# Kernel tuning notes

Measured on AMD Instinct MI355X. Metric: run time of the kernel, lower is better.

The kernel has to match this reference:

```python
import jax, jax.numpy as jnp
import numpy as np

NUM_FREQUENCIES = 6  # K = 2F+1 = 13


def fourier_basis(times, num_frequencies):
    # times: [N] -> basis: [N, 2F+1] = [1, sin(2^j*pi*t), cos(2^j*pi*t)]
    freqs = (2.0 ** jnp.arange(num_frequencies, dtype=times.dtype)) * jnp.pi  # [F]
    ang = times[:, None] * freqs[None, :]  # [N, F]
    ones = jnp.ones_like(times)[:, None]
    return jnp.concatenate([ones, jnp.sin(ang), jnp.cos(ang)], axis=-1)  # [N, K]


def setup_inputs() -> dict:
    key = jax.random.key(0)
    k1, k2, k3 = jax.random.split(key, 3)
    N, num_videos, embedding_dim = 400000, 128, 64
    times = jax.random.uniform(k1, (N,), dtype=jnp.float32)
    video_ids = jax.random.randint(k2, (N,), 0, num_videos, dtype=jnp.int32)
    weights = jax.random.normal(k3, (num_videos, embedding_dim, 2 * NUM_FREQUENCIES + 1), dtype=jnp.float32)
    return {"times": times, "video_ids": video_ids, "weights": weights}


def reference(times, video_ids, weights):
    basis = fourier_basis(times, NUM_FREQUENCIES)          # [N, K]
    w = weights[video_ids]                                  # gather: [N, D, K]
    return jnp.einsum('nk,ndk->nd', basis, w)               # [N, D]
```

## Files before the change

### kernel.cpp

```cpp
#include <hip/hip_runtime.h>
#include <math.h>

#define V 128
#define D 64
#define K 13

#define CHUNK 2048
#define SORT_BLOCK 256
#define NB 256
#define BSTRIDE 20

__global__ void zero_kernel(int* __restrict__ gcount) {
    gcount[threadIdx.x] = 0;
}

__global__ __launch_bounds__(256) void sort_kernel(const int* __restrict__ ids, int n,
                                                   int* __restrict__ gcount,
                                                   int* __restrict__ sorted, int cap) {
    __shared__ int h[V];
    __shared__ int r[V];
    __shared__ int lb[V];
    int tid = threadIdx.x;
    if (tid < V) { h[tid] = 0; r[tid] = 0; }
    __syncthreads();
    int base = blockIdx.x * CHUNK;
    int4 reg[CHUNK / (SORT_BLOCK * 4)];
#pragma unroll
    for (int j = 0; j < CHUNK / (SORT_BLOCK * 4); ++j) {
        int i = base + (j * SORT_BLOCK + tid) * 4;
        if (i < n) {
            reg[j] = *(const int4*)(ids + i);
            atomicAdd(&h[reg[j].x], 1);
            atomicAdd(&h[reg[j].y], 1);
            atomicAdd(&h[reg[j].z], 1);
            atomicAdd(&h[reg[j].w], 1);
        }
    }
    __syncthreads();
    if (tid < V) lb[tid] = atomicAdd(&gcount[tid], h[tid]);
    __syncthreads();
#pragma unroll
    for (int j = 0; j < CHUNK / (SORT_BLOCK * 4); ++j) {
        int i = base + (j * SORT_BLOCK + tid) * 4;
        if (i < n) {
            int4 v4 = reg[j];
            int p0 = lb[v4.x] + atomicAdd(&r[v4.x], 1);
            int p1 = lb[v4.y] + atomicAdd(&r[v4.y], 1);
            int p2 = lb[v4.z] + atomicAdd(&r[v4.z], 1);
            int p3 = lb[v4.w] + atomicAdd(&r[v4.w], 1);
            if (p0 < cap) sorted[v4.x * cap + p0] = i;
            if (p1 < cap) sorted[v4.y * cap + p1] = i + 1;
            if (p2 < cap) sorted[v4.z * cap + p2] = i + 2;
            if (p3 < cap) sorted[v4.w * cap + p3] = i + 3;
        }
    }
}

__global__ __launch_bounds__(256) void compute_kernel(const float* __restrict__ times,
                                                      const float* __restrict__ weights,
                                                      const int* __restrict__ sorted,
                                                      const int* __restrict__ gcount,
                                                      float* __restrict__ out,
                                                      int cap, int bpb) {
    int v = (int)(blockIdx.x) / bpb;
    int blk = (int)(blockIdx.x) - v * bpb;
    int cnt = gcount[v];
    if (cnt > cap) cnt = cap;
    int start = blk * NB;
    int valid = cnt - start;
    if (valid <= 0) return;
    if (valid > NB) valid = NB;

    __shared__ float basis[NB * BSTRIDE];
    int tid = threadIdx.x;
    int lane = tid & 63;

    float w[K];
    {
        const float* wp = weights + (v * D + lane) * K;
#pragma unroll
        for (int k = 0; k < K; ++k) w[k] = wp[k];
    }

    if (tid < valid) {
        int idx = sorted[v * cap + start + tid];
        float t = times[idx];
        float s, c;
        __sincosf(3.14159265358979323846f * t, &s, &c);
        float sj[6], cj[6];
        sj[0] = s; cj[0] = c;
#pragma unroll
        for (int j = 1; j < 6; ++j) {
            sj[j] = 2.0f * sj[j - 1] * cj[j - 1];
            cj[j] = 1.0f - 2.0f * sj[j - 1] * sj[j - 1];
        }
        float* bb = &basis[tid * BSTRIDE];
        ((float4*)bb)[0] = make_float4(1.0f, sj[0], sj[1], sj[2]);
        ((float4*)bb)[1] = make_float4(sj[3], sj[4], sj[5], cj[0]);
        ((float4*)bb)[2] = make_float4(cj[1], cj[2], cj[3], cj[4]);
        *(float2*)(bb + 12) = make_float2(cj[5], __int_as_float(idx));
    }
    __syncthreads();

    int wave = tid >> 6;
    int i0 = wave * 64;
    int iend = valid - i0;
    iend = iend < 0 ? 0 : (iend > 64 ? 64 : iend);

    auto body = [&](int i) {
        const float* bb = &basis[(i0 + i) * BSTRIDE];
        float4 b0 = ((const float4*)bb)[0];
        float4 b1 = ((const float4*)bb)[1];
        float4 b2 = ((const float4*)bb)[2];
        float2 b3 = *(const float2*)(bb + 12);
        int idx = __float_as_int(b3.y);
        float acc = ((b0.x * w[0] + b0.y * w[1]) + (b0.z * w[2] + b0.w * w[3]))
                  + ((b1.x * w[4] + b1.y * w[5]) + (b1.z * w[6] + b1.w * w[7]))
                  + (((b2.x * w[8] + b2.y * w[9]) + (b2.z * w[10] + b2.w * w[11]))
                     + b3.x * w[12]);
        __builtin_nontemporal_store(acc, &out[(long)idx * D + lane]);
    };

    if (iend == 64) {
#pragma unroll 4
        for (int i = 0; i < 64; ++i) body(i);
    } else {
        for (int i = 0; i < iend; ++i) body(i);
    }
}

extern "C" void kernel_launch(void* const* d_in, const int* in_sizes, int n_in,
                              void* d_out, int out_size, void* d_ws, size_t ws_size,
                              hipStream_t stream) {
    const float* times = (const float*)d_in[0];
    const int* ids = (const int*)d_in[1];
    const float* weights = (const float*)d_in[2];
    float* out = (float*)d_out;
    int n = in_sizes[0];

    int* gcount = (int*)d_ws;
    int* sorted = gcount + V;
    long avail = (long)(ws_size / 4) - V;
    int cap = (int)(avail / V);
    if (cap > 4096) cap = 4096;

    zero_kernel<<<1, V, 0, stream>>>(gcount);

    int nblk = (n + CHUNK - 1) / CHUNK;
    sort_kernel<<<nblk, SORT_BLOCK, 0, stream>>>(ids, n, gcount, sorted, cap);

    int bpb = (cap + NB - 1) / NB;
    compute_kernel<<<V * bpb, 256, 0, stream>>>(times, weights, sorted, gcount, out, cap, bpb);
}
```

Baseline: 130.7 us.

## Fuse zero, sort and compute kernels into one cooperative persistent kernel

Replaces the three separate launches (zero counters, bucket sort by video id, per-video compute) with a single cooperative kernel of 1024 persistent blocks that uses grid-wide syncs between phases and grid-strided loops over chunks and jobs. The aim is to remove launch overhead and inter-kernel gaps. If the cooperative launch fails, it falls back to the old three-kernel path. The grid syncs add their own cost, and capping the grid at 1024 blocks with occupancy 4 may reduce parallelism in the compute phase.

Result: slower. 297.6 us (+127.8%).

```diff
diff --git a/kernel.cpp b/kernel.cpp
--- a/kernel.cpp
+++ b/kernel.cpp
@@ -1,18 +1,142 @@
 #include <hip/hip_runtime.h>
+#include <hip/hip_cooperative_groups.h>
 #include <math.h>
+
+namespace cg = cooperative_groups;
 
 #define V 128
 #define D 64
 #define K 13
 
+#define NBLK 1024
 #define CHUNK 2048
 #define SORT_BLOCK 256
 #define NB 256
 #define BSTRIDE 20
 
-__global__ void zero_kernel(int* __restrict__ gcount) {
-    gcount[threadIdx.x] = 0;
-}
+__global__ __launch_bounds__(256, 4) void fused_kernel(
+    const float* __restrict__ times, const int* __restrict__ ids,
+    const float* __restrict__ weights, float* __restrict__ out,
+    int* __restrict__ gcount, int* __restrict__ sorted,
+    int n, int cap, int bpb, int nchunk, int njobs)
+{
+    __shared__ int h[V];
+    __shared__ int r[V];
+    __shared__ int lb[V];
+    __shared__ float basis[NB * BSTRIDE];
+
+    int tid = threadIdx.x;
+    cg::grid_group grid = cg::this_grid();
+
+    if (blockIdx.x == 0 && tid < V) gcount[tid] = 0;
+    grid.sync();
+
+    for (int c = blockIdx.x; c < nchunk; c += NBLK) {
+        if (tid < V) { h[tid] = 0; r[tid] = 0; }
+        __syncthreads();
+        int base = c * CHUNK;
+        int4 reg[CHUNK / (SORT_BLOCK * 4)];
+#pragma unroll
+        for (int j = 0; j < CHUNK / (SORT_BLOCK * 4); ++j) {
+            int i = base + (j * SORT_BLOCK + tid) * 4;
+            if (i < n) {
+                reg[j] = *(const int4*)(ids + i);
+                atomicAdd(&h[reg[j].x], 1);
+                atomicAdd(&h[reg[j].y], 1);
+                atomicAdd(&h[reg[j].z], 1);
+                atomicAdd(&h[reg[j].w], 1);
+            }
+        }
+        __syncthreads();
+        if (tid < V) lb[tid] = atomicAdd(&gcount[tid], h[tid]);
+        __syncthreads();
+#pragma unroll
+        for (int j = 0; j < CHUNK / (SORT_BLOCK * 4); ++j) {
+            int i = base + (j * SORT_BLOCK + tid) * 4;
+            if (i < n) {
+                int4 v4 = reg[j];
+                int p0 = lb[v4.x] + atomicAdd(&r[v4.x], 1);
+                int p1 = lb[v4.y] + atomicAdd(&r[v4.y], 1);
+                int p2 = lb[v4.z] + atomicAdd(&r[v4.z], 1);
+                int p3 = lb[v4.w] + atomicAdd(&r[v4.w], 1);
+                if (p0 < cap) sorted[v4.x * cap + p0] = i;
+                if (p1 < cap) sorted[v4.y * cap + p1] = i + 1;
+                if (p2 < cap) sorted[v4.z * cap + p2] = i + 2;
+                if (p3 < cap) sorted[v4.w * cap + p3] = i + 3;
+            }
+        }
+        __syncthreads();
+    }
+    grid.sync();
+
+    int lane = tid & 63;
+    int wave = tid >> 6;
+    for (int job = blockIdx.x; job < njobs; job += NBLK) {
+        int v = job / bpb;
+        int blk = job - v * bpb;
+        int cnt = gcount[v];
+        if (cnt > cap) cnt = cap;
+        int start = blk * NB;
+        int valid = cnt - start;
+        if (valid <= 0) continue;
+        if (valid > NB) valid = NB;
+
+        float w[K];
+        {
+            const float* wp = weights + (v * D + lane) * K;
+#pragma unroll
+            for (int k = 0; k < K; ++k) w[k] = wp[k];
+        }
+
+        if (tid < valid) {
+            int idx = sorted[v * cap + start + tid];
+            float t = times[idx];
+            float s, c;
+            __sincosf(3.14159265358979323846f * t, &s, &c);
+            float sj[6], cj[6];
+            sj[0] = s; cj[0] = c;
+#pragma unroll
+            for (int j = 1; j < 6; ++j) {
+                sj[j] = 2.0f * sj[j - 1] * cj[j - 1];
+                cj[j] = 1.0f - 2.0f * sj[j - 1] * sj[j - 1];
+            }
+            float* bb = &basis[tid * BSTRIDE];
+            ((float4*)bb)[0] = make_float4(1.0f, sj[0], sj[1], sj[2]);
+            ((float4*)bb)[1] = make_float4(sj[3], sj[4], sj[5], cj[0]);
+            ((float4*)bb)[2] = make_float4(cj[1], cj[2], cj[3], cj[4]);
+            *(float2*)(bb + 12) = make_float2(cj[5], __int_as_float(idx));
+        }
+        __syncthreads();
+
+        int i0 = wave * 64;
+        int iend = valid - i0;
+        iend = iend < 0 ? 0 : (iend > 64 ? 64 : iend);
+
+        auto body = [&](int i) {
+            const float* bb = &basis[(i0 + i) * BSTRIDE];
+            float4 b0 = ((const float4*)bb)[0];
+            float4 b1 = ((const float4*)bb)[1];
+            float4 b2 = ((const float4*)bb)[2];
+            float2 b3 = *(const float2*)(bb + 12);
+            int idx = __float_as_int(b3.y);
+            float acc = ((b0.x * w[0] + b0.y * w[1]) + (b0.z * w[2] + b0.w * w[3]))
+                      + ((b1.x * w[4] + b1.y * w[5]) + (b1.z * w[6] + b1.w * w[7]))
+                      + (((b2.x * w[8] + b2.y * w[9]) + (b2.z * w[10] + b2.w * w[11]))
+                         + b3.x * w[12]);
+            __builtin_nontemporal_store(acc, &out[(long)idx * D + lane]);
+        };
+
+        if (iend == 64) {
+#pragma unroll 4
+            for (int i = 0; i < 64; ++i) body(i);
+        } else {
+            for (int i = 0; i < iend; ++i) body(i);
+        }
+        __syncthreads();
+    }
+}
+
+__global__ void zero_kernel(int* __restrict__ gcount) { gcount[threadIdx.x] = 0; }
 
 __global__ __launch_bounds__(256) void sort_kernel(const int* __restrict__ ids, int n,
                                                    int* __restrict__ gcount,
@@ -144,11 +268,18 @@
     int cap = (int)(avail / V);
     if (cap > 4096) cap = 4096;
 
-    zero_kernel<<<1, V, 0, stream>>>(gcount);
-
-    int nblk = (n + CHUNK - 1) / CHUNK;
-    sort_kernel<<<nblk, SORT_BLOCK, 0, stream>>>(ids, n, gcount, sorted, cap);
-
+    int nchunk = (n + CHUNK - 1) / CHUNK;
     int bpb = (cap + NB - 1) / NB;
-    compute_kernel<<<V * bpb, 256, 0, stream>>>(times, weights, sorted, gcount, out, cap, bpb);
-}
+    int njobs = V * bpb;
+
+    void* args[] = { (void*)&times, (void*)&ids, (void*)&weights, (void*)&out,
+                     (void*)&gcount, (void*)&sorted,
+                     (void*)&n, (void*)&cap, (void*)&bpb, (void*)&nchunk, (void*)&njobs };
+    hipError_t err = hipLaunchCooperativeKernel((const void*)fused_kernel,
+                                                dim3(NBLK), dim3(256), args, 0, stream);
+    if (err != hipSuccess) {
+        zero_kernel<<<1, V, 0, stream>>>(gcount);
+        sort_kernel<<<nchunk, SORT_BLOCK, 0, stream>>>(ids, n, gcount, sorted, cap);
+        compute_kernel<<<njobs, 256, 0, stream>>>(times, weights, sorted, gcount, out, cap, bpb);
+    }
+}
```

## Replace bucket-sort pipeline with single kernel gathering per-row weights from cache

Applied to the files above, without the earlier changes.

Drops the zero/sort kernels and the per-video bucketed compute. Each block now handles 256 consecutive rows. It builds the Fourier basis in shared memory and, for every row, reads that row's video id as a wave-uniform scalar and loads 13 weights per lane from the 425KB weight table, which should stay in cache. Output writes become fully contiguous, and two launches plus the atomics and scattered index traffic go away. In exchange each row now needs 13 cached weight loads, where before the weights sat in registers.

After: 251.7 us. 1.93x slower.

```diff
diff --git a/kernel.cpp b/kernel.cpp
--- a/kernel.cpp
+++ b/kernel.cpp
@@ -5,86 +5,21 @@
 #define D 64
 #define K 13
 
-#define CHUNK 2048
-#define SORT_BLOCK 256
 #define NB 256
-#define BSTRIDE 20
+#define BSTRIDE 16
 
-__global__ void zero_kernel(int* __restrict__ gcount) {
-    gcount[threadIdx.x] = 0;
-}
-
-__global__ __launch_bounds__(256) void sort_kernel(const int* __restrict__ ids, int n,
-                                                   int* __restrict__ gcount,
-                                                   int* __restrict__ sorted, int cap) {
-    __shared__ int h[V];
-    __shared__ int r[V];
-    __shared__ int lb[V];
-    int tid = threadIdx.x;
-    if (tid < V) { h[tid] = 0; r[tid] = 0; }
-    __syncthreads();
-    int base = blockIdx.x * CHUNK;
-    int4 reg[CHUNK / (SORT_BLOCK * 4)];
-#pragma unroll
-    for (int j = 0; j < CHUNK / (SORT_BLOCK * 4); ++j) {
-        int i = base + (j * SORT_BLOCK + tid) * 4;
-        if (i < n) {
-            reg[j] = *(const int4*)(ids + i);
-            atomicAdd(&h[reg[j].x], 1);
-            atomicAdd(&h[reg[j].y], 1);
-            atomicAdd(&h[reg[j].z], 1);
-            atomicAdd(&h[reg[j].w], 1);
-        }
-    }
-    __syncthreads();
-    if (tid < V) lb[tid] = atomicAdd(&gcount[tid], h[tid]);
-    __syncthreads();
-#pragma unroll
-    for (int j = 0; j < CHUNK / (SORT_BLOCK * 4); ++j) {
-        int i = base + (j * SORT_BLOCK + tid) * 4;
-        if (i < n) {
-            int4 v4 = reg[j];
-            int p0 = lb[v4.x] + atomicAdd(&r[v4.x], 1);
-            int p1 = lb[v4.y] + atomicAdd(&r[v4.y], 1);
-            int p2 = lb[v4.z] + atomicAdd(&r[v4.z], 1);
-            int p3 = lb[v4.w] + atomicAdd(&r[v4.w], 1);
-            if (p0 < cap) sorted[v4.x * cap + p0] = i;
-            if (p1 < cap) sorted[v4.y * cap + p1] = i + 1;
-            if (p2 < cap) sorted[v4.z * cap + p2] = i + 2;
-            if (p3 < cap) sorted[v4.w * cap + p3] = i + 3;
-        }
-    }
-}
-
-__global__ __launch_bounds__(256) void compute_kernel(const float* __restrict__ times,
-                                                      const float* __restrict__ weights,
-                                                      const int* __restrict__ sorted,
-                                                      const int* __restrict__ gcount,
-                                                      float* __restrict__ out,
-                                                      int cap, int bpb) {
-    int v = (int)(blockIdx.x) / bpb;
-    int blk = (int)(blockIdx.x) - v * bpb;
-    int cnt = gcount[v];
-    if (cnt > cap) cnt = cap;
-    int start = blk * NB;
-    int valid = cnt - start;
-    if (valid <= 0) return;
-    if (valid > NB) valid = NB;
-
+__global__ __launch_bounds__(256) void fourier_kernel(
+    const float* __restrict__ times, const int* __restrict__ ids,
+    const float* __restrict__ weights, float* __restrict__ out, int n)
+{
     __shared__ float basis[NB * BSTRIDE];
     int tid = threadIdx.x;
-    int lane = tid & 63;
+    int gbase = blockIdx.x * NB;
+    int g = gbase + tid;
 
-    float w[K];
-    {
-        const float* wp = weights + (v * D + lane) * K;
-#pragma unroll
-        for (int k = 0; k < K; ++k) w[k] = wp[k];
-    }
-
-    if (tid < valid) {
-        int idx = sorted[v * cap + start + tid];
-        float t = times[idx];
+    if (g < n) {
+        float t = times[g];
+        int vid = ids[g];
         float s, c;
         __sincosf(3.14159265358979323846f * t, &s, &c);
         float sj[6], cj[6];
@@ -98,27 +33,34 @@
         ((float4*)bb)[0] = make_float4(1.0f, sj[0], sj[1], sj[2]);
         ((float4*)bb)[1] = make_float4(sj[3], sj[4], sj[5], cj[0]);
         ((float4*)bb)[2] = make_float4(cj[1], cj[2], cj[3], cj[4]);
-        *(float2*)(bb + 12) = make_float2(cj[5], __int_as_float(idx));
+        ((float2*)bb)[6] = make_float2(cj[5], __int_as_float(vid));
     }
     __syncthreads();
 
+    int lane = tid & 63;
     int wave = tid >> 6;
     int i0 = wave * 64;
-    int iend = valid - i0;
+    int iend = n - gbase - i0;
     iend = iend < 0 ? 0 : (iend > 64 ? 64 : iend);
+    int laneK = lane * K;
 
     auto body = [&](int i) {
         const float* bb = &basis[(i0 + i) * BSTRIDE];
         float4 b0 = ((const float4*)bb)[0];
         float4 b1 = ((const float4*)bb)[1];
         float4 b2 = ((const float4*)bb)[2];
-        float2 b3 = *(const float2*)(bb + 12);
-        int idx = __float_as_int(b3.y);
-        float acc = ((b0.x * w[0] + b0.y * w[1]) + (b0.z * w[2] + b0.w * w[3]))
-                  + ((b1.x * w[4] + b1.y * w[5]) + (b1.z * w[6] + b1.w * w[7]))
-                  + (((b2.x * w[8] + b2.y * w[9]) + (b2.z * w[10] + b2.w * w[11]))
-                     + b3.x * w[12]);
-        __builtin_nontemporal_store(acc, &out[(long)idx * D + lane]);
+        float2 b3 = ((const float2*)bb)[6];
+        int v = __builtin_amdgcn_readfirstlane(__float_as_int(b3.y));
+        const float* wp = weights + v * (D * K) + laneK;
+        float w0 = wp[0], w1 = wp[1], w2 = wp[2], w3 = wp[3];
+        float w4 = wp[4], w5 = wp[5], w6 = wp[6], w7 = wp[7];
+        float w8 = wp[8], w9 = wp[9], w10 = wp[10], w11 = wp[11];
+        float w12 = wp[12];
+        float acc = ((b0.x * w0 + b0.y * w1) + (b0.z * w2 + b0.w * w3))
+                  + ((b1.x * w4 + b1.y * w5) + (b1.z * w6 + b1.w * w7))
+                  + (((b2.x * w8 + b2.y * w9) + (b2.z * w10 + b2.w * w11))
+                     + b3.x * w12);
+        __builtin_nontemporal_store(acc, &out[(long)(gbase + i0 + i) * D + lane]);
     };
 
     if (iend == 64) {
@@ -137,18 +79,8 @@
     const float* weights = (const float*)d_in[2];
     float* out = (float*)d_out;
     int n = in_sizes[0];
+    (void)d_ws; (void)ws_size;
 
-    int* gcount = (int*)d_ws;
-    int* sorted = gcount + V;
-    long avail = (long)(ws_size / 4) - V;
-    int cap = (int)(avail / V);
-    if (cap > 4096) cap = 4096;
-
-    zero_kernel<<<1, V, 0, stream>>>(gcount);
-
-    int nblk = (n + CHUNK - 1) / CHUNK;
-    sort_kernel<<<nblk, SORT_BLOCK, 0, stream>>>(ids, n, gcount, sorted, cap);
-
-    int bpb = (cap + NB - 1) / NB;
-    compute_kernel<<<V * bpb, 256, 0, stream>>>(times, weights, sorted, gcount, out, cap, bpb);
+    int nblk = (n + NB - 1) / NB;
+    fourier_kernel<<<nblk, 256, 0, stream>>>(times, ids, weights, out, n);
 }
```
